# Kernel tuning notes

Hardware: AMD Instinct MI355X
Metric: run time of the kernel (lower is better)

Reference implementation:

```python
import jax, jax.numpy as jnp
import numpy as np

D_MODEL = 1024
N_HEADS = 16


def setup_inputs() -> dict:
    key = jax.random.key(0)
    ks = jax.random.split(key, 5)
    B, T, C = 4, 2048, D_MODEL
    x = jax.random.normal(ks[0], (B, T, C), dtype=jnp.float32)
    s = 1.0 / np.sqrt(C)
    W_attn = jax.random.normal(ks[1], (C, 3 * C), dtype=jnp.float32) * s
    b_attn = jnp.zeros((3 * C,), dtype=jnp.float32)
    W_proj = jax.random.normal(ks[2], (C, C), dtype=jnp.float32) * s
    b_proj = jnp.zeros((C,), dtype=jnp.float32)
    return {"x": x, "W_attn": W_attn, "b_attn": b_attn, "W_proj": W_proj, "b_proj": b_proj}


def reference(x, W_attn, b_attn, W_proj, b_proj):
    B, T, C = x.shape
    H = N_HEADS
    hd = C // H
    qkv = x @ W_attn + b_attn                      # [B,T,3C]
    q, k, v = jnp.split(qkv, 3, axis=-1)
    # reshape to [B,H,T,hd]
    q = q.reshape(B, T, H, hd).transpose(0, 2, 1, 3)
    k = k.reshape(B, T, H, hd).transpose(0, 2, 1, 3)
    v = v.reshape(B, T, H, hd).transpose(0, 2, 1, 3)
    scale = 1.0 / jnp.sqrt(jnp.asarray(hd, dtype=x.dtype))
    aff = jnp.einsum('bhqd,bhkd->bhqk', q, k) * scale   # [B,H,T,T]
    causal = jnp.tril(jnp.ones((T, T), dtype=bool))
    aff = jnp.where(causal, aff, jnp.asarray(-jnp.inf, dtype=aff.dtype))
    p = jax.nn.softmax(aff, axis=-1)
    y = jnp.einsum('bhqk,bhkd->bhqd', p, v)             # [B,H,T,hd]
    y = y.transpose(0, 2, 1, 3).reshape(B, T, C)
    return y @ W_proj + b_proj
```

## Files before the change

kernel.cpp:

```cpp
#include <hip/hip_runtime.h>
#include <stdint.h>
#include <math.h>

typedef __attribute__((ext_vector_type(8))) __bf16 bf16x8;
typedef __attribute__((ext_vector_type(4))) __bf16 bf16x4;
typedef __attribute__((ext_vector_type(4))) float f32x4;

#define MFMA16(A, B, C) __builtin_amdgcn_mfma_f32_16x16x32_bf16((A), (B), (C), 0, 0, 0)

#if defined(__has_builtin)
#if __has_builtin(__builtin_amdgcn_exp2f)
#define EXP2(x) __builtin_amdgcn_exp2f(x)
#else
#define EXP2(x) exp2f(x)
#endif
#else
#define EXP2(x) exp2f(x)
#endif

static constexpr int kT  = 2048;
static constexpr int kC  = 1024;
static constexpr int kHD = 64;
#define QSCALE 0.1803368801111204f

__device__ __forceinline__ void g2l16(const void* g, void* l) {
  __builtin_amdgcn_global_load_lds(
      (const __attribute__((address_space(1))) uint32_t*)g,
      (__attribute__((address_space(3))) uint32_t*)l, 16, 0, 0);
}

__global__ __launch_bounds__(256) void k_convert_x(const float* __restrict__ x,
                                                   __bf16* __restrict__ xb) {
  int i = (blockIdx.x * 256 + threadIdx.x) * 4;
  f32x4 v = *(const f32x4*)(x + i);
  bf16x4 o;
  o[0] = (__bf16)v[0]; o[1] = (__bf16)v[1]; o[2] = (__bf16)v[2]; o[3] = (__bf16)v[3];
  *(bf16x4*)(xb + i) = o;
}

__global__ __launch_bounds__(256) void k_transpose_w(const float* __restrict__ src,
                                                     __bf16* __restrict__ dst, int N) {
  __shared__ float t[32][33];
  int k0 = blockIdx.x * 32, n0 = blockIdx.y * 32;
  int c = threadIdx.x & 31, r = threadIdx.x >> 5;
#pragma unroll
  for (int i = 0; i < 4; ++i)
    t[r + i * 8][c] = src[(size_t)(k0 + r + i * 8) * N + n0 + c];
  __syncthreads();
#pragma unroll
  for (int i = 0; i < 4; ++i)
    dst[(size_t)(n0 + r + i * 8) * 1024 + k0 + c] = (__bf16)t[c][r + i * 8];
}

__global__ __launch_bounds__(256) void k_transpose_v(const __bf16* __restrict__ src,
                                                     __bf16* __restrict__ dst) {
  __shared__ __bf16 t[32][33];
  const int t0 = blockIdx.x * 32, d0 = blockIdx.y * 32;
  const size_t base = (size_t)blockIdx.z * kT * kHD;
  int c = threadIdx.x & 31, r = threadIdx.x >> 5;
#pragma unroll
  for (int i = 0; i < 4; ++i)
    t[r + i * 8][c] = src[base + (size_t)(t0 + r + i * 8) * kHD + d0 + c];
  __syncthreads();
#pragma unroll
  for (int i = 0; i < 4; ++i)
    dst[base + (size_t)(d0 + r + i * 8) * kT + t0 + c] = t[c][r + i * 8];
}

static constexpr int GK = 1024;
static constexpr int GNT = GK / 32;

template <int MODE>
__global__ __launch_bounds__(512, 2) void k_gemm(const __bf16* __restrict__ A,
                                                 const __bf16* __restrict__ Bw,
                                                 const float* __restrict__ bias,
                                                 __bf16* __restrict__ qo,
                                                 __bf16* __restrict__ ko,
                                                 __bf16* __restrict__ vo,
                                                 float* __restrict__ out) {
  __shared__ __bf16 As[4][128 * 32];
  __shared__ __bf16 Bs[4][256 * 32];

  const int tid = threadIdx.x;
  const int wave = tid >> 6, lane = tid & 63;
  const int lo = lane & 15, hi = lane >> 4;
  const int wr = wave >> 2, wc = wave & 3;

  const int nwg = (int)gridDim.x;
  const int id = (int)blockIdx.x;
  const int wg = (id & 7) * (nwg >> 3) + (id >> 3);
  const int bm = wg & 63, bn = wg >> 6;
  const int m0 = bm * 128, n0 = bn * 256;

  const int rA = tid >> 2, gA = tid & 3;
  const int gsw = gA ^ ((rA >> 1) & 3);
  const __bf16* ga = A + (size_t)(m0 + rA) * GK + gsw * 8;
  const __bf16* gb = Bw + (size_t)(n0 + rA) * GK + gsw * 8;

  const int fsw = (hi ^ ((lo >> 1) & 3)) * 8;
  const int offA = (wr * 64 + lo) * 32 + fsw;
  const int offB = (wc * 64 + lo) * 32 + fsw;

  f32x4 acc[4][4] = {};

#define GSTAGE(jt, bufi)                                                      \
  {                                                                           \
    g2l16(ga + (jt) * 32, &As[(bufi)][wave * 512]);                           \
    g2l16(gb + (jt) * 32, &Bs[(bufi)][wave * 512]);                           \
    g2l16(gb + (jt) * 32 + (size_t)128 * GK, &Bs[(bufi)][4096 + wave * 512]); \
  }

  GSTAGE(0, 0);
  GSTAGE(1, 1);
  GSTAGE(2, 2);
  asm volatile("s_waitcnt vmcnt(6)" ::: "memory");
  __builtin_amdgcn_s_barrier();

  for (int j = 0; j < GNT; ++j) {
    const __bf16* Ab = &As[j & 3][0];
    const __bf16* Bb = &Bs[j & 3][0];
    bf16x8 af[4], bfr[4];
#pragma unroll
    for (int m = 0; m < 4; ++m) af[m] = *(const bf16x8*)&Ab[offA + m * 512];
#pragma unroll
    for (int n = 0; n < 4; ++n) bfr[n] = *(const bf16x8*)&Bb[offB + n * 512];
    if (j < GNT - 3) GSTAGE(j + 3, (j + 3) & 3);
    __builtin_amdgcn_s_barrier();
    __builtin_amdgcn_sched_barrier(0);
    __builtin_amdgcn_s_setprio(1);
#pragma unroll
    for (int m = 0; m < 4; ++m)
#pragma unroll
      for (int n = 0; n < 4; ++n)
        acc[m][n] = MFMA16(af[m], bfr[n], acc[m][n]);
    __builtin_amdgcn_s_setprio(0);
    __builtin_amdgcn_sched_barrier(0);
    if (j < GNT - 3) {
      asm volatile("s_waitcnt vmcnt(6)" ::: "memory");
    } else if (j == GNT - 3) {
      asm volatile("s_waitcnt vmcnt(3)" ::: "memory");
    } else if (j == GNT - 2) {
      asm volatile("s_waitcnt vmcnt(0)" ::: "memory");
    }
    if (j < GNT - 1) __builtin_amdgcn_s_barrier();
  }
#undef GSTAGE

  if (MODE == 0) {
#pragma unroll
    for (int nj = 0; nj < 4; ++nj) {
      int gn = n0 + wc * 64 + nj * 16 + lo;
      float bv = bias[gn];
      int which = gn >> 10;
      int c = gn & 1023;
      int hh = c >> 6, d = c & 63;
#pragma unroll
      for (int mi = 0; mi < 4; ++mi) {
        int gm = m0 + wr * 64 + mi * 16 + hi * 4;
#pragma unroll
        for (int r = 0; r < 4; ++r) {
          int m = gm + r;
          int bb = m >> 11, t = m & 2047;
          float val = acc[mi][nj][r] + bv;
          size_t idx = (((size_t)(bb * 16 + hh)) * 2048 + t) * 64 + d;
          if (which == 0)
            qo[idx] = (__bf16)(val * QSCALE);
          else if (which == 1)
            ko[idx] = (__bf16)val;
          else
            vo[idx] = (__bf16)val;
        }
      }
    }
  } else {
#pragma unroll
    for (int nj = 0; nj < 4; ++nj) {
      int gn = n0 + wc * 64 + nj * 16 + lo;
      float bv = bias[gn];
#pragma unroll
      for (int mi = 0; mi < 4; ++mi) {
        int gm = m0 + wr * 64 + mi * 16 + hi * 4;
#pragma unroll
        for (int r = 0; r < 4; ++r)
          out[(size_t)(gm + r) * 1024 + gn] = acc[mi][nj][r] + bv;
      }
    }
  }
}

__global__ __launch_bounds__(256, 4) void k_flash(const __bf16* __restrict__ qb,
                                                  const __bf16* __restrict__ kb,
                                                  const __bf16* __restrict__ vt,
                                                  __bf16* __restrict__ ob) {
  __shared__ __bf16 Ks[2][64 * 64];
  __shared__ __bf16 Vs[2][64 * 64];
  __shared__ __bf16 Ps[4][16 * 64];

  const int id = (int)blockIdx.y * 16 + (int)blockIdx.x;
  const int xcd = id & 7, jj = id >> 3;
  const int bh = (jj & 7) * 8 + xcd;
  const int xs = jj >> 3;
  const int b = bh >> 4, h = bh & 15;
  const int tid = threadIdx.x, wave = tid >> 6, lane = tid & 63;
  const int lo = lane & 15, hi = lane >> 4;

  const int qrow[2] = { (31 - xs) * 64 + wave * 16, xs * 64 + wave * 16 };

  bf16x8 qf[2][2];
#pragma unroll
  for (int rg = 0; rg < 2; ++rg) {
    const __bf16* Qp = qb + ((size_t)bh * kT + qrow[rg]) * kHD;
    qf[rg][0] = *(const bf16x8*)(Qp + lo * kHD + hi * 8);
    qf[rg][1] = *(const bf16x8*)(Qp + lo * kHD + 32 + hi * 8);
  }

  bf16x8 onesf;
#pragma unroll
  for (int e = 0; e < 8; ++e) onesf[e] = (lo == 0) ? (__bf16)1.0f : (__bf16)0.0f;

  f32x4 acc[2][4] = {};
  f32x4 accsum[2] = {};

  const __bf16* Kbase = kb + (size_t)bh * kT * kHD;
  const __bf16* Vbase = vt + (size_t)bh * kHD * kT;

  int srcK[2], srcV[2];
#pragma unroll
  for (int p = 0; p < 2; ++p) {
    int g = wave * 64 + lane + p * 256;
    int r = g >> 3, c = g & 7;
    int cs = c ^ (r & 7);
    srcK[p] = r * kHD + cs * 8;
    srcV[p] = r * kT + cs * 8;
  }
  const int sw0 = (hi ^ (lo & 7)) * 8;
  const int sw1 = ((hi + 4) ^ (lo & 7)) * 8;
  const int psw0 = (hi ^ (lo >> 1)) * 8;
  const int psw1 = ((hi + 4) ^ (lo >> 1)) * 8;

  const int nt = 32 - xs;

#pragma unroll
  for (int p = 0; p < 2; ++p) {
    g2l16(Kbase + srcK[p], &Ks[0][wave * 512 + p * 2048]);
    g2l16(Vbase + srcV[p], &Vs[0][wave * 512 + p * 2048]);
  }

  for (int it = 0; it < nt; ++it) {
    const int kt = it * 64;
    const int pb = it & 1;
    const bool both = (it <= xs);

    __syncthreads();

    if (it + 1 < nt) {
      const int kn = kt + 64;
#pragma unroll
      for (int p = 0; p < 2; ++p) {
        g2l16(Kbase + kn * kHD + srcK[p], &Ks[1 - pb][wave * 512 + p * 2048]);
        g2l16(Vbase + kn + srcV[p],       &Vs[1 - pb][wave * 512 + p * 2048]);
      }
    }

    const __bf16* Kt = &Ks[pb][0];
    const __bf16* Vt = &Vs[pb][0];
    f32x4 s[2][4];
    __builtin_amdgcn_s_setprio(1);
#pragma unroll
    for (int j = 0; j < 4; ++j) {
      const int row = (j * 16 + lo) * 64;
      bf16x8 kf0 = *(const bf16x8*)&Kt[row + sw0];
      bf16x8 kf1 = *(const bf16x8*)&Kt[row + sw1];
      f32x4 z = {};
      z = MFMA16(qf[0][0], kf0, z);
      z = MFMA16(qf[0][1], kf1, z);
      s[0][j] = z;
      if (both) {
        f32x4 z1 = {};
        z1 = MFMA16(qf[1][0], kf0, z1);
        z1 = MFMA16(qf[1][1], kf1, z1);
        s[1][j] = z1;
      }
    }
    __builtin_amdgcn_s_setprio(0);

    bf16x8 pf[2][2];
#pragma unroll
    for (int rg = 0; rg < 2; ++rg) {
      if (rg == 1 && !both) break;
      const int q0 = qrow[rg] + hi * 4;
      if (kt + 63 > q0) {
#pragma unroll
        for (int j = 0; j < 4; ++j)
#pragma unroll
          for (int r = 0; r < 4; ++r)
            if (kt + j * 16 + lo > q0 + r) s[rg][j][r] = -INFINITY;
      }
#pragma unroll
      for (int j = 0; j < 4; ++j)
#pragma unroll
        for (int r = 0; r < 4; ++r)
          s[rg][j][r] = EXP2(s[rg][j][r]);
      __bf16* Pw = &Ps[wave][0];
#pragma unroll
      for (int j = 0; j < 4; ++j)
#pragma unroll
        for (int r = 0; r < 4; ++r) {
          const int q = hi * 4 + r;
          Pw[q * 64 + (((j * 2 + (lo >> 3)) ^ (q >> 1)) * 8) + (lo & 7)] =
              (__bf16)s[rg][j][r];
        }
      pf[rg][0] = *(const bf16x8*)&Pw[lo * 64 + psw0];
      pf[rg][1] = *(const bf16x8*)&Pw[lo * 64 + psw1];
    }

    __builtin_amdgcn_s_setprio(1);
    accsum[0] = MFMA16(pf[0][0], onesf, accsum[0]);
    accsum[0] = MFMA16(pf[0][1], onesf, accsum[0]);
    if (both) {
      accsum[1] = MFMA16(pf[1][0], onesf, accsum[1]);
      accsum[1] = MFMA16(pf[1][1], onesf, accsum[1]);
    }
#pragma unroll
    for (int jd = 0; jd < 4; ++jd) {
      const int row = (jd * 16 + lo) * 64;
      bf16x8 vf0 = *(const bf16x8*)&Vt[row + sw0];
      bf16x8 vf1 = *(const bf16x8*)&Vt[row + sw1];
      acc[0][jd] = MFMA16(pf[0][0], vf0, acc[0][jd]);
      acc[0][jd] = MFMA16(pf[0][1], vf1, acc[0][jd]);
      if (both) {
        acc[1][jd] = MFMA16(pf[1][0], vf0, acc[1][jd]);
        acc[1][jd] = MFMA16(pf[1][1], vf1, acc[1][jd]);
      }
    }
    __builtin_amdgcn_s_setprio(0);
  }

#pragma unroll
  for (int rg = 0; rg < 2; ++rg) {
    float inv[4];
#pragma unroll
    for (int r = 0; r < 4; ++r)
      inv[r] = 1.0f / __shfl(accsum[rg][r], hi * 16, 64);
    __bf16* Op = ob + ((size_t)b * kT + qrow[rg]) * kC + h * kHD;
#pragma unroll
    for (int jd = 0; jd < 4; ++jd)
#pragma unroll
      for (int r = 0; r < 4; ++r)
        Op[(hi * 4 + r) * kC + jd * 16 + lo] = (__bf16)(acc[rg][jd][r] * inv[r]);
  }
}

extern "C" void kernel_launch(void* const* d_in, const int* in_sizes, int n_in,
                              void* d_out, int out_size, void* d_ws, size_t ws_size,
                              hipStream_t stream) {
  const float* x      = (const float*)d_in[0];
  const float* W_attn = (const float*)d_in[1];
  const float* b_attn = (const float*)d_in[2];
  const float* W_proj = (const float*)d_in[3];
  const float* b_proj = (const float*)d_in[4];
  float* out = (float*)d_out;

  char* ws = (char*)d_ws;
  __bf16* xb  = (__bf16*)(ws + 0);
  __bf16* vtb = (__bf16*)(ws + 0);
  __bf16* wab = (__bf16*)(ws + 16777216);
  __bf16* wpb = (__bf16*)(ws + 23068672);
  __bf16* qbf = (__bf16*)(ws + 25165824);
  __bf16* kbf = (__bf16*)(ws + 41943040);
  __bf16* vbf = (__bf16*)(ws + 58720256);
  __bf16* ob  = (__bf16*)(ws + 58720256);

  k_convert_x<<<8192, 256, 0, stream>>>(x, xb);
  k_transpose_w<<<dim3(32, 96), 256, 0, stream>>>(W_attn, wab, 3072);
  k_transpose_w<<<dim3(32, 32), 256, 0, stream>>>(W_proj, wpb, 1024);
  k_gemm<0><<<dim3(768), 512, 0, stream>>>(xb, wab, b_attn, qbf, kbf, vbf, nullptr);
  k_transpose_v<<<dim3(64, 2, 64), 256, 0, stream>>>(vbf, vtb);
  k_flash<<<dim3(16, 64), 256, 0, stream>>>(qbf, kbf, vtb, ob);
  k_gemm<1><<<dim3(256), 512, 0, stream>>>(ob, wpb, b_proj, nullptr, nullptr, nullptr, out);
}
```

Baseline: 288.9 us.

## Fuse V transpose into QKV GEMM epilogue and retile GEMM to 128x128

The QKV GEMM epilogue now writes V directly in transposed [B,H,hd,T] layout with 4-wide bf16 stores, so the separate k_transpose_v kernel and its extra round trip through memory are removed. The GEMM is also retiled from a 128x256 block with 512 threads and a 4-stage LDS ring to a 128x128 block with 256 threads and a 3-stage ring. This doubles the grid and aims for 3 blocks per CU. Workspace aliasing is rearranged so the attention output reuses the x buffer. The smaller tile lowers per-block operand reuse, and the loop now has one barrier per iteration instead of two.

```diff
diff --git a/kernel.cpp b/kernel.cpp
--- a/kernel.cpp
+++ b/kernel.cpp
@@ -52,50 +52,38 @@
     dst[(size_t)(n0 + r + i * 8) * 1024 + k0 + c] = (__bf16)t[c][r + i * 8];
 }
 
-__global__ __launch_bounds__(256) void k_transpose_v(const __bf16* __restrict__ src,
-                                                     __bf16* __restrict__ dst) {
-  __shared__ __bf16 t[32][33];
-  const int t0 = blockIdx.x * 32, d0 = blockIdx.y * 32;
-  const size_t base = (size_t)blockIdx.z * kT * kHD;
-  int c = threadIdx.x & 31, r = threadIdx.x >> 5;
-#pragma unroll
-  for (int i = 0; i < 4; ++i)
-    t[r + i * 8][c] = src[base + (size_t)(t0 + r + i * 8) * kHD + d0 + c];
-  __syncthreads();
-#pragma unroll
-  for (int i = 0; i < 4; ++i)
-    dst[base + (size_t)(d0 + r + i * 8) * kT + t0 + c] = t[c][r + i * 8];
-}
-
 static constexpr int GK = 1024;
 static constexpr int GNT = GK / 32;
 
 template <int MODE>
-__global__ __launch_bounds__(512, 2) void k_gemm(const __bf16* __restrict__ A,
+__global__ __launch_bounds__(256, 3) void k_gemm(const __bf16* __restrict__ A,
                                                  const __bf16* __restrict__ Bw,
                                                  const float* __restrict__ bias,
                                                  __bf16* __restrict__ qo,
                                                  __bf16* __restrict__ ko,
                                                  __bf16* __restrict__ vo,
                                                  float* __restrict__ out) {
-  __shared__ __bf16 As[4][128 * 32];
-  __shared__ __bf16 Bs[4][256 * 32];
+  __shared__ __bf16 As[3][128 * 32];
+  __shared__ __bf16 Bs[3][128 * 32];
 
   const int tid = threadIdx.x;
   const int wave = tid >> 6, lane = tid & 63;
   const int lo = lane & 15, hi = lane >> 4;
-  const int wr = wave >> 2, wc = wave & 3;
-
+  const int wr = wave & 1, wc = wave >> 1;
+
+  constexpr int NBN = (MODE == 0) ? 24 : 8;
   const int nwg = (int)gridDim.x;
   const int id = (int)blockIdx.x;
   const int wg = (id & 7) * (nwg >> 3) + (id >> 3);
-  const int bm = wg & 63, bn = wg >> 6;
-  const int m0 = bm * 128, n0 = bn * 256;
-
-  const int rA = tid >> 2, gA = tid & 3;
-  const int gsw = gA ^ ((rA >> 1) & 3);
-  const __bf16* ga = A + (size_t)(m0 + rA) * GK + gsw * 8;
-  const __bf16* gb = Bw + (size_t)(n0 + rA) * GK + gsw * 8;
+  const int bm = wg / NBN, bn = wg % NBN;
+  const int m0 = bm * 128, n0 = bn * 128;
+
+  const int rG0 = tid >> 2, gG0 = (tid & 3) ^ ((rG0 >> 1) & 3);
+  const int rG1 = (tid + 256) >> 2, gG1 = ((tid + 256) & 3) ^ ((rG1 >> 1) & 3);
+  const __bf16* gaA0 = A + (size_t)(m0 + rG0) * GK + gG0 * 8;
+  const __bf16* gaA1 = A + (size_t)(m0 + rG1) * GK + gG1 * 8;
+  const __bf16* gbB0 = Bw + (size_t)(n0 + rG0) * GK + gG0 * 8;
+  const __bf16* gbB1 = Bw + (size_t)(n0 + rG1) * GK + gG1 * 8;
 
   const int fsw = (hi ^ ((lo >> 1) & 3)) * 8;
   const int offA = (wr * 64 + lo) * 32 + fsw;
@@ -103,30 +91,30 @@
 
   f32x4 acc[4][4] = {};
 
-#define GSTAGE(jt, bufi)                                                      \
-  {                                                                           \
-    g2l16(ga + (jt) * 32, &As[(bufi)][wave * 512]);                           \
-    g2l16(gb + (jt) * 32, &Bs[(bufi)][wave * 512]);                           \
-    g2l16(gb + (jt) * 32 + (size_t)128 * GK, &Bs[(bufi)][4096 + wave * 512]); \
+#define GSTAGE(jt, bufi)                                  \
+  {                                                       \
+    g2l16(gaA0 + (jt) * 32, &As[(bufi)][tid * 8]);        \
+    g2l16(gaA1 + (jt) * 32, &As[(bufi)][2048 + tid * 8]); \
+    g2l16(gbB0 + (jt) * 32, &Bs[(bufi)][tid * 8]);        \
+    g2l16(gbB1 + (jt) * 32, &Bs[(bufi)][2048 + tid * 8]); \
   }
 
   GSTAGE(0, 0);
   GSTAGE(1, 1);
-  GSTAGE(2, 2);
-  asm volatile("s_waitcnt vmcnt(6)" ::: "memory");
+  asm volatile("s_waitcnt vmcnt(4)" ::: "memory");
   __builtin_amdgcn_s_barrier();
-
+  __builtin_amdgcn_sched_barrier(0);
+
+  int rb = 0, rs = 2;
   for (int j = 0; j < GNT; ++j) {
-    const __bf16* Ab = &As[j & 3][0];
-    const __bf16* Bb = &Bs[j & 3][0];
+    const __bf16* Ab = &As[rb][0];
+    const __bf16* Bb = &Bs[rb][0];
+    if (j < GNT - 2) GSTAGE(j + 2, rs);
     bf16x8 af[4], bfr[4];
 #pragma unroll
     for (int m = 0; m < 4; ++m) af[m] = *(const bf16x8*)&Ab[offA + m * 512];
 #pragma unroll
     for (int n = 0; n < 4; ++n) bfr[n] = *(const bf16x8*)&Bb[offB + n * 512];
-    if (j < GNT - 3) GSTAGE(j + 3, (j + 3) & 3);
-    __builtin_amdgcn_s_barrier();
-    __builtin_amdgcn_sched_barrier(0);
     __builtin_amdgcn_s_setprio(1);
 #pragma unroll
     for (int m = 0; m < 4; ++m)
@@ -134,15 +122,17 @@
       for (int n = 0; n < 4; ++n)
         acc[m][n] = MFMA16(af[m], bfr[n], acc[m][n]);
     __builtin_amdgcn_s_setprio(0);
-    __builtin_amdgcn_sched_barrier(0);
-    if (j < GNT - 3) {
-      asm volatile("s_waitcnt vmcnt(6)" ::: "memory");
-    } else if (j == GNT - 3) {
-      asm volatile("s_waitcnt vmcnt(3)" ::: "memory");
+    if (j < GNT - 2) {
+      asm volatile("s_waitcnt vmcnt(4)" ::: "memory");
     } else if (j == GNT - 2) {
       asm volatile("s_waitcnt vmcnt(0)" ::: "memory");
     }
-    if (j < GNT - 1) __builtin_amdgcn_s_barrier();
+    if (j < GNT - 1) {
+      __builtin_amdgcn_s_barrier();
+      __builtin_amdgcn_sched_barrier(0);
+    }
+    rb = (rb == 2) ? 0 : rb + 1;
+    rs = (rs == 2) ? 0 : rs + 1;
   }
 #undef GSTAGE
 
@@ -157,18 +147,22 @@
 #pragma unroll
       for (int mi = 0; mi < 4; ++mi) {
         int gm = m0 + wr * 64 + mi * 16 + hi * 4;
-#pragma unroll
-        for (int r = 0; r < 4; ++r) {
-          int m = gm + r;
-          int bb = m >> 11, t = m & 2047;
-          float val = acc[mi][nj][r] + bv;
-          size_t idx = (((size_t)(bb * 16 + hh)) * 2048 + t) * 64 + d;
-          if (which == 0)
-            qo[idx] = (__bf16)(val * QSCALE);
-          else if (which == 1)
-            ko[idx] = (__bf16)val;
-          else
-            vo[idx] = (__bf16)val;
+        int bb = gm >> 11, t0 = gm & 2047;
+        if (which == 2) {
+          bf16x4 vv;
+#pragma unroll
+          for (int r = 0; r < 4; ++r) vv[r] = (__bf16)(acc[mi][nj][r] + bv);
+          *(bf16x4*)(vo + ((size_t)(bb * 16 + hh) * 64 + d) * 2048 + t0) = vv;
+        } else {
+#pragma unroll
+          for (int r = 0; r < 4; ++r) {
+            float val = acc[mi][nj][r] + bv;
+            size_t idx = (((size_t)(bb * 16 + hh)) * 2048 + (t0 + r)) * 64 + d;
+            if (which == 0)
+              qo[idx] = (__bf16)(val * QSCALE);
+            else
+              ko[idx] = (__bf16)val;
+          }
         }
       }
     }
@@ -363,19 +357,17 @@
 
   char* ws = (char*)d_ws;
   __bf16* xb  = (__bf16*)(ws + 0);
-  __bf16* vtb = (__bf16*)(ws + 0);
+  __bf16* ob  = (__bf16*)(ws + 0);
   __bf16* wab = (__bf16*)(ws + 16777216);
   __bf16* wpb = (__bf16*)(ws + 23068672);
   __bf16* qbf = (__bf16*)(ws + 25165824);
   __bf16* kbf = (__bf16*)(ws + 41943040);
-  __bf16* vbf = (__bf16*)(ws + 58720256);
-  __bf16* ob  = (__bf16*)(ws + 58720256);
+  __bf16* vtb = (__bf16*)(ws + 58720256);
 
   k_convert_x<<<8192, 256, 0, stream>>>(x, xb);
   k_transpose_w<<<dim3(32, 96), 256, 0, stream>>>(W_attn, wab, 3072);
   k_transpose_w<<<dim3(32, 32), 256, 0, stream>>>(W_proj, wpb, 1024);
-  k_gemm<0><<<dim3(768), 512, 0, stream>>>(xb, wab, b_attn, qbf, kbf, vbf, nullptr);
-  k_transpose_v<<<dim3(64, 2, 64), 256, 0, stream>>>(vbf, vtb);
+  k_gemm<0><<<dim3(1536), 256, 0, stream>>>(xb, wab, b_attn, qbf, kbf, vtb, nullptr);
   k_flash<<<dim3(16, 64), 256, 0, stream>>>(qbf, kbf, vtb, ob);
-  k_gemm<1><<<dim3(256), 512, 0, stream>>>(ob, wpb, b_proj, nullptr, nullptr, nullptr, out);
-}
+  k_gemm<1><<<dim3(512), 256, 0, stream>>>(ob, wpb, b_proj, nullptr, nullptr, nullptr, out);
+}
```

After: 261.5 us. 9.5% less time.
